# Kernel optimization log

Measured on AMD Instinct MI355X. Metric: run time of the kernel, lower is better.

The kernel has to match this reference:

```python
import jax, jax.numpy as jnp
import numpy as np

NEG_SLOPE = 0.01  # torch F.leaky_relu default

def leaky_relu(x):
    return jnp.where(x >= 0, x, NEG_SLOPE * x)

def setup_inputs() -> dict:
    key = jax.random.key(0)
    ks = jax.random.split(key, 16)
    N, D, H, L = 2048, 512, 256, 16
    # normalized-adjacency-like matrix: row sums ~0.5 to keep activations sane
    A_hat = jax.random.uniform(ks[0], (N, N), dtype=jnp.float32) / N
    X = jax.random.normal(ks[1], (N, D), dtype=jnp.float32)
    eps = jax.random.normal(ks[2], (N, L), dtype=jnp.float32)
    def lin(k, fan_out, fan_in):
        s = 1.0 / np.sqrt(fan_in)
        kw, kb = jax.random.split(k)
        W = jax.random.uniform(kw, (fan_out, fan_in), minval=-s, maxval=s, dtype=jnp.float32)
        b = jax.random.uniform(kb, (fan_out,), minval=-s, maxval=s, dtype=jnp.float32)
        return W, b
    W1, b1 = lin(ks[3], H, D)          # gcn1
    Wmu, bmu = lin(ks[4], L, H)        # gcn2_mu
    Wlv, blv = lin(ks[5], L, H)        # gcn2_logvar
    Wd1, bd1 = lin(ks[6], 2 * L, 2 * L)  # decoder_fc1
    Wd2, bd2 = lin(ks[7], 1, 2 * L)      # decoder_fc2
    return {"A_hat": A_hat, "X": X, "eps": eps,
            "W1": W1, "b1": b1, "Wmu": Wmu, "bmu": bmu,
            "Wlv": Wlv, "blv": blv, "Wd1": Wd1, "bd1": bd1,
            "Wd2": Wd2, "bd2": bd2}

def reference(A_hat, X, eps, W1, b1, Wmu, bmu, Wlv, blv, Wd1, bd1, Wd2, bd2):
    L = Wmu.shape[0]
    # --- encode: two GCN layers (A_hat @ X) @ W.T + b ---
    Hh = leaky_relu((A_hat @ X) @ W1.T + b1)           # [N, H]
    AH = A_hat @ Hh                                    # [N, H]
    mu = AH @ Wmu.T + bmu                              # [N, L]
    logvar = AH @ Wlv.T + blv                          # [N, L]
    # --- reparameterize ---
    Z = mu + eps * jnp.exp(0.5 * logvar)               # [N, L]
    # --- decode: pairwise MLP on concat(Z_i, Z_j), vectorized ---
    # fc1(concat(Zi,Zj)) = Zi @ Wd1[:, :L].T + Zj @ Wd1[:, L:].T + bd1
    P = Z @ Wd1[:, :L].T                               # [N, 2L]
    Q = Z @ Wd1[:, L:].T                               # [N, 2L]
    h = leaky_relu(P[:, None, :] + Q[None, :, :] + bd1)  # [N, N, 2L]
    A_pred = jax.nn.sigmoid(jnp.einsum('nmh,h->nm', h, Wd2[0]) + bd2[0])  # [N, N]
    return (A_pred, mu, logvar)
```

## Files before the change

### kernel.cpp

```cpp
#include <hip/hip_runtime.h>

#define NNODE 2048
#define DD    512
#define HHID  256
#define LLAT  16
#define H2    32

typedef __attribute__((ext_vector_type(8))) short  short8;
typedef __attribute__((ext_vector_type(4))) float  f32x4;

__device__ __forceinline__ unsigned short f2bf(float x) {
    unsigned int u = __float_as_uint(x);
    unsigned int r = (u + 0x7fffu + ((u >> 16) & 1u)) >> 16;
    return (unsigned short)r;
}
__device__ __forceinline__ float bf2f(unsigned short u) {
    return __uint_as_float(((unsigned int)u) << 16);
}

__global__ __launch_bounds__(256) void t0_cvt(const float* __restrict__ A,
                                              const float* __restrict__ X,
                                              const float* __restrict__ W1,
                                              unsigned short* __restrict__ Abf,
                                              unsigned short* __restrict__ Xbf,
                                              unsigned short* __restrict__ W1bf) {
    const int NT = 1343488;
    for (int v = blockIdx.x * 256 + threadIdx.x; v < NT; v += gridDim.x * 256) {
        const float* src; unsigned short* dst; int off;
        if (v < 1048576)      { src = A;  dst = Abf;  off = v; }
        else if (v < 1310720) { src = X;  dst = Xbf;  off = v - 1048576; }
        else                  { src = W1; dst = W1bf; off = v - 1310720; }
        float4 f = ((const float4*)src)[off];
        short4 h;
        h.x = (short)f2bf(f.x); h.y = (short)f2bf(f.y);
        h.z = (short)f2bf(f.z); h.w = (short)f2bf(f.w);
        ((short4*)dst)[off] = h;
    }
}

__global__ __launch_bounds__(256) void t1_full(const unsigned short* __restrict__ W1bf,
                                               const unsigned short* __restrict__ Xbf,
                                               unsigned short* __restrict__ XWt) {
    __shared__ __align__(16) unsigned short Ab[32][72];
    __shared__ __align__(16) unsigned short Bb[32][72];
    const int tid = threadIdx.x;
    const int n0 = blockIdx.x * 32;
    const int h0 = blockIdx.y * 32;
    const int lane = tid & 63, wave = tid >> 6;
    const int wm = wave >> 1, wn = wave & 1;
    const int lm = lane & 15, lk = (lane >> 4) * 8;
    const int sr = tid >> 3, sc = (tid & 7) * 8;
    f32x4 acc = {};
    for (int it = 0; it < 8; ++it) {
        int kk = it * 64;
        *(uint4*)&Ab[sr][sc] = *(const uint4*)(W1bf + (size_t)(h0 + sr) * DD + kk + sc);
        *(uint4*)&Bb[sr][sc] = *(const uint4*)(Xbf  + (size_t)(n0 + sr) * DD + kk + sc);
        __syncthreads();
        #pragma unroll
        for (int ko = 0; ko < 2; ++ko) {
            short8 a = *(const short8*)&Ab[wm * 16 + lm][ko * 32 + lk];
            short8 b = *(const short8*)&Bb[wn * 16 + lm][ko * 32 + lk];
            acc = __builtin_amdgcn_mfma_f32_16x16x32_bf16(a, b, acc, 0, 0, 0);
        }
        __syncthreads();
    }
    #pragma unroll
    for (int r = 0; r < 4; ++r) {
        int row = h0 + wm * 16 + (lane >> 4) * 4 + r;
        int col = n0 + wn * 16 + lm;
        XWt[(size_t)row * NNODE + col] = f2bf(acc[r]);
    }
}

__global__ __launch_bounds__(256) void t2_mfma(const unsigned short* __restrict__ Abf,
                                               const unsigned short* __restrict__ XWt,
                                               float* __restrict__ Hp) {
    __shared__ __align__(16) unsigned short Ab[64][40];
    __shared__ __align__(16) unsigned short Bb[64][40];
    const int tid = threadIdx.x;
    const int m0 = blockIdx.x * 64;
    const int n0 = blockIdx.y * 64;
    const int ks = blockIdx.z;
    const int lane = tid & 63, wave = tid >> 6;
    const int wm = wave >> 1, wn = wave & 1;
    const int lm = lane & 15, lk = (lane >> 4) * 8;
    const int sr = tid >> 2, sc = (tid & 3) * 8;
    f32x4 acc[2][2] = {};
    for (int it = 0; it < 16; ++it) {
        int kk = ks * 512 + it * 32;
        *(uint4*)&Ab[sr][sc] = *(const uint4*)(Abf + (size_t)(m0 + sr) * NNODE + kk + sc);
        *(uint4*)&Bb[sr][sc] = *(const uint4*)(XWt + (size_t)(n0 + sr) * NNODE + kk + sc);
        __syncthreads();
        short8 a0 = *(const short8*)&Ab[wm * 32 + lm][lk];
        short8 a1 = *(const short8*)&Ab[wm * 32 + 16 + lm][lk];
        short8 b0 = *(const short8*)&Bb[wn * 32 + lm][lk];
        short8 b1 = *(const short8*)&Bb[wn * 32 + 16 + lm][lk];
        acc[0][0] = __builtin_amdgcn_mfma_f32_16x16x32_bf16(a0, b0, acc[0][0], 0, 0, 0);
        acc[0][1] = __builtin_amdgcn_mfma_f32_16x16x32_bf16(a0, b1, acc[0][1], 0, 0, 0);
        acc[1][0] = __builtin_amdgcn_mfma_f32_16x16x32_bf16(a1, b0, acc[1][0], 0, 0, 0);
        acc[1][1] = __builtin_amdgcn_mfma_f32_16x16x32_bf16(a1, b1, acc[1][1], 0, 0, 0);
        __syncthreads();
    }
    float* outp = Hp + (size_t)ks * 524288;
    #pragma unroll
    for (int mi = 0; mi < 2; ++mi)
        #pragma unroll
        for (int ni = 0; ni < 2; ++ni)
            #pragma unroll
            for (int r = 0; r < 4; ++r) {
                int row = m0 + wm * 32 + mi * 16 + (lane >> 4) * 4 + r;
                int col = n0 + wn * 32 + ni * 16 + lm;
                outp[(size_t)row * HHID + col] = acc[mi][ni][r];
            }
}

__global__ __launch_bounds__(256) void t3h(const float* __restrict__ Hp,
                                           const float* __restrict__ b1,
                                           const float* __restrict__ Wmu,
                                           const float* __restrict__ Wlv,
                                           unsigned short* __restrict__ Gt) {
    __shared__ float Hs[8][260];
    __shared__ float Ws[32][260];
    const int tid = threadIdx.x;
    const int n0 = blockIdx.x * 8;
    #pragma unroll
    for (int s = 0; s < 8; ++s) {
        int idx = tid + s * 256;
        int row = idx >> 6, c = (idx & 63) * 4;
        const float* src = (row < 16) ? (Wmu + (size_t)row * HHID)
                                      : (Wlv + (size_t)(row - 16) * HHID);
        *(float4*)&Ws[row][c] = *(const float4*)(src + c);
    }
    {
        int r = tid >> 5, seg = tid & 31;
        int dcol = seg * 8;
        const float* base = Hp + (size_t)(n0 + r) * HHID + dcol;
        #pragma unroll
        for (int q = 0; q < 2; ++q) {
            float4 a = *(const float4*)(base + q * 4);
            float4 b = *(const float4*)(base + 524288 + q * 4);
            float4 c = *(const float4*)(base + 1048576 + q * 4);
            float4 e = *(const float4*)(base + 1572864 + q * 4);
            float4 bb = *(const float4*)(b1 + dcol + q * 4);
            float4 s;
            s.x = (a.x + b.x) + (c.x + e.x) + bb.x;
            s.y = (a.y + b.y) + (c.y + e.y) + bb.y;
            s.z = (a.z + b.z) + (c.z + e.z) + bb.z;
            s.w = (a.w + b.w) + (c.w + e.w) + bb.w;
            s.x = fmaxf(s.x, 0.01f * s.x);
            s.y = fmaxf(s.y, 0.01f * s.y);
            s.z = fmaxf(s.z, 0.01f * s.z);
            s.w = fmaxf(s.w, 0.01f * s.w);
            Hs[r][dcol + q * 4 + 0] = bf2f(f2bf(s.x));
            Hs[r][dcol + q * 4 + 1] = bf2f(f2bf(s.y));
            Hs[r][dcol + q * 4 + 2] = bf2f(f2bf(s.z));
            Hs[r][dcol + q * 4 + 3] = bf2f(f2bf(s.w));
        }
    }
    __syncthreads();
    const int r = tid >> 5, j = tid & 31;
    float acc = 0.f;
    #pragma unroll 8
    for (int d4 = 0; d4 < 64; ++d4) {
        float4 a = *(const float4*)&Hs[r][d4 * 4];
        float4 b = *(const float4*)&Ws[j][d4 * 4];
        acc += a.x * b.x + a.y * b.y + a.z * b.z + a.w * b.w;
    }
    Gt[(size_t)j * NNODE + n0 + r] = f2bf(acc);
}

__global__ __launch_bounds__(256) void t4_mfma(const unsigned short* __restrict__ Abf,
                                               const unsigned short* __restrict__ Gt,
                                               float* __restrict__ Mp) {
    __shared__ __align__(16) unsigned short Ab[64][40];
    __shared__ __align__(16) unsigned short Bb[32][40];
    const int tid = threadIdx.x;
    const int m0 = blockIdx.x * 64;
    const int ks = blockIdx.y;
    const int lane = tid & 63, wave = tid >> 6;
    const int lm = lane & 15, lk = (lane >> 4) * 8;
    const int sr = tid >> 2, sc = (tid & 3) * 8;
    f32x4 acc[2] = {};
    for (int it = 0; it < 8; ++it) {
        int kk = ks * 256 + it * 32;
        *(uint4*)&Ab[sr][sc] = *(const uint4*)(Abf + (size_t)(m0 + sr) * NNODE + kk + sc);
        if (tid < 128) {
            int row = tid >> 2, c = (tid & 3) * 8;
            *(uint4*)&Bb[row][c] = *(const uint4*)(Gt + (size_t)row * NNODE + kk + c);
        }
        __syncthreads();
        short8 a  = *(const short8*)&Ab[wave * 16 + lm][lk];
        short8 b0 = *(const short8*)&Bb[lm][lk];
        short8 b1 = *(const short8*)&Bb[16 + lm][lk];
        acc[0] = __builtin_amdgcn_mfma_f32_16x16x32_bf16(a, b0, acc[0], 0, 0, 0);
        acc[1] = __builtin_amdgcn_mfma_f32_16x16x32_bf16(a, b1, acc[1], 0, 0, 0);
        __syncthreads();
    }
    float* outp = Mp + (size_t)ks * 65536;
    #pragma unroll
    for (int ni = 0; ni < 2; ++ni)
        #pragma unroll
        for (int r = 0; r < 4; ++r) {
            int row = m0 + wave * 16 + (lane >> 4) * 4 + r;
            int col = ni * 16 + lm;
            outp[(size_t)row * H2 + col] = acc[ni][r];
        }
}

__global__ __launch_bounds__(256) void t5_z(const float* __restrict__ Mp,
                                            const float* __restrict__ bmu,
                                            const float* __restrict__ blv,
                                            const float* __restrict__ eps,
                                            const float* __restrict__ Wd1,
                                            const float* __restrict__ bd1,
                                            const float* __restrict__ Wd2,
                                            float* __restrict__ out_mu,
                                            float* __restrict__ out_lv,
                                            float* __restrict__ Pp,
                                            float* __restrict__ Qq,
                                            float* __restrict__ WP,
                                            float* __restrict__ WQ) {
    __shared__ float Zs[16][16];
    __shared__ float Psh[16][32];
    __shared__ float Qsh[16][32];
    const int tid = threadIdx.x;
    const int n0 = blockIdx.x * 16;
    {
        int nl = tid >> 4, l = tid & 15;
        int n = n0 + nl;
        float m = bmu[l], lv = blv[l];
        #pragma unroll
        for (int s = 0; s < 8; ++s) {
            m  += Mp[(size_t)s * 65536 + (size_t)n * H2 + l];
            lv += Mp[(size_t)s * 65536 + (size_t)n * H2 + 16 + l];
        }
        out_mu[(size_t)n * LLAT + l] = m;
        out_lv[(size_t)n * LLAT + l] = lv;
        Zs[nl][l] = m + eps[(size_t)n * LLAT + l] * __expf(0.5f * lv);
    }
    __syncthreads();
    #pragma unroll
    for (int p = 0; p < 2; ++p) {
        int idx = tid + p * 256;
        int nl = idx >> 5, o = idx & 31;
        int n = n0 + nl;
        float ap = bd1[o], aq = 0.f;
        #pragma unroll
        for (int l = 0; l < 16; ++l) {
            float z = Zs[nl][l];
            ap = fmaf(z, Wd1[o * H2 + l],      ap);
            aq = fmaf(z, Wd1[o * H2 + 16 + l], aq);
        }
        Pp[(size_t)n * H2 + o] = ap;
        Qq[(size_t)n * H2 + o] = aq;
        Psh[nl][o] = ap;
        Qsh[nl][o] = aq;
    }
    __syncthreads();
    if (tid < 32) {
        int nl = tid & 15, sel = tid >> 4;
        float a = 0.f;
        if (sel == 0) {
            #pragma unroll
            for (int o = 0; o < 32; ++o) a = fmaf(Wd2[o], Psh[nl][o], a);
            WP[n0 + nl] = a;
        } else {
            #pragma unroll
            for (int o = 0; o < 32; ++o) a = fmaf(Wd2[o], Qsh[nl][o], a);
            WQ[n0 + nl] = a;
        }
    }
}

__global__ __launch_bounds__(256) void t6_dec(const float* __restrict__ Pp,
                                              const float* __restrict__ Qq,
                                              const float* __restrict__ WP,
                                              const float* __restrict__ WQ,
                                              const float* __restrict__ Wd2,
                                              const float* __restrict__ bd2,
                                              float* __restrict__ Apred) {
    __shared__ float Qt[32][68];
    __shared__ float Ws2[32];
    __shared__ float WQs[64];
    const int tid = threadIdx.x;
    const int j0 = blockIdx.x * 64, i0 = blockIdx.y * 16;
    #pragma unroll
    for (int s = 0; s < 8; ++s) {
        int idx = tid + s * 256;
        int j = idx >> 5, o = idx & 31;
        Qt[o][j] = Qq[(size_t)(j0 + j) * H2 + o];
    }
    if (tid < 32) Ws2[tid] = Wd2[tid];
    if (tid >= 64 && tid < 128) WQs[tid - 64] = WQ[j0 + tid - 64];
    const int i = i0 + (tid >> 4);
    const int jq = tid & 15;
    float p[32];
    const float4* P4 = (const float4*)(Pp + (size_t)i * H2);
    #pragma unroll
    for (int c = 0; c < 8; ++c) {
        float4 v = P4[c];
        p[c * 4] = v.x; p[c * 4 + 1] = v.y; p[c * 4 + 2] = v.z; p[c * 4 + 3] = v.w;
    }
    const float WPi = WP[i];
    __syncthreads();
    f32x4 acc = {0.f, 0.f, 0.f, 0.f};
    #pragma unroll
    for (int o = 0; o < 32; ++o) {
        float4 q = *(const float4*)&Qt[o][jq * 4];
        float w = Ws2[o], po = p[o];
        acc[0] = fmaf(w, fabsf(po + q.x), acc[0]);
        acc[1] = fmaf(w, fabsf(po + q.y), acc[1]);
        acc[2] = fmaf(w, fabsf(po + q.z), acc[2]);
        acc[3] = fmaf(w, fabsf(po + q.w), acc[3]);
    }
    float4 wq = *(const float4*)&WQs[jq * 4];
    const float base = fmaf(0.505f, WPi, bd2[0]);
    float4 r;
    float l0 = fmaf(0.505f, wq.x, fmaf(0.495f, acc[0], base));
    float l1 = fmaf(0.505f, wq.y, fmaf(0.495f, acc[1], base));
    float l2 = fmaf(0.505f, wq.z, fmaf(0.495f, acc[2], base));
    float l3 = fmaf(0.505f, wq.w, fmaf(0.495f, acc[3], base));
    r.x = 1.f / (1.f + __expf(-l0));
    r.y = 1.f / (1.f + __expf(-l1));
    r.z = 1.f / (1.f + __expf(-l2));
    r.w = 1.f / (1.f + __expf(-l3));
    *(float4*)(Apred + (size_t)i * NNODE + j0 + jq * 4) = r;
}

extern "C" void kernel_launch(void* const* d_in, const int* in_sizes, int n_in,
                              void* d_out, int out_size, void* d_ws, size_t ws_size,
                              hipStream_t stream) {
    const float* A   = (const float*)d_in[0];
    const float* X   = (const float*)d_in[1];
    const float* eps = (const float*)d_in[2];
    const float* W1  = (const float*)d_in[3];
    const float* b1  = (const float*)d_in[4];
    const float* Wmu = (const float*)d_in[5];
    const float* bmu = (const float*)d_in[6];
    const float* Wlv = (const float*)d_in[7];
    const float* blv = (const float*)d_in[8];
    const float* Wd1 = (const float*)d_in[9];
    const float* bd1 = (const float*)d_in[10];
    const float* Wd2 = (const float*)d_in[11];
    const float* bd2 = (const float*)d_in[12];
    float* out = (float*)d_out;
    char* ws = (char*)d_ws;

    unsigned short* Abf  = (unsigned short*)(ws);
    unsigned short* Xbf  = (unsigned short*)(ws + 8388608);
    unsigned short* W1bf = (unsigned short*)(ws + 10485760);
    unsigned short* XWt  = (unsigned short*)(ws + 10747904);
    float*          Hp   = (float*)(ws + 11796480);
    unsigned short* Gt   = (unsigned short*)(ws + 20185088);
    float*          Mp   = (float*)(ws + 20316160);
    float*          Pp   = (float*)(ws + 22413312);
    float*          Qq   = (float*)(ws + 22675456);
    float*          WP   = (float*)(ws + 22937600);
    float*          WQ   = (float*)(ws + 22945792);

    float* out_mu = out + (size_t)NNODE * NNODE;
    float* out_lv = out_mu + NNODE * LLAT;

    t0_cvt <<<2048,            256, 0, stream>>>(A, X, W1, Abf, Xbf, W1bf);
    t1_full<<<dim3(64, 8),     256, 0, stream>>>(W1bf, Xbf, XWt);
    t2_mfma<<<dim3(32, 4, 4),  256, 0, stream>>>(Abf, XWt, Hp);
    t3h    <<<256,             256, 0, stream>>>(Hp, b1, Wmu, Wlv, Gt);
    t4_mfma<<<dim3(32, 8),     256, 0, stream>>>(Abf, Gt, Mp);
    t5_z   <<<128,             256, 0, stream>>>(Mp, bmu, blv, eps, Wd1, bd1, Wd2,
                                                 out_mu, out_lv, Pp, Qq, WP, WQ);
    t6_dec <<<dim3(32, 128),   256, 0, stream>>>(Pp, Qq, WP, WQ, Wd2, bd2, out);
}
```

Measured before the change: 137.1 us.

## Replace split-K GEMM with full-K tile, fusing bias and leaky ReLU

The second GEMM (A_hat times XW) no longer splits K four ways into fp32 partial buffers that a later kernel sums. Each block now covers the full K=2048 on a smaller 32x32 tile and applies bias and leaky ReLU in its epilogue, writing bf16 H directly. Global loads are register-prefetched one iteration ahead. This removes the 8MB fp32 partial writes and reads. In exchange, each block runs a longer serial K loop and does less work per LDS load, with 512 blocks instead of 512 split-K blocks.

```diff
diff --git a/kernel.cpp b/kernel.cpp
--- a/kernel.cpp
+++ b/kernel.cpp
@@ -72,53 +72,55 @@
     }
 }
 
-__global__ __launch_bounds__(256) void t2_mfma(const unsigned short* __restrict__ Abf,
+__global__ __launch_bounds__(256) void t2_full(const unsigned short* __restrict__ Abf,
                                                const unsigned short* __restrict__ XWt,
-                                               float* __restrict__ Hp) {
-    __shared__ __align__(16) unsigned short Ab[64][40];
-    __shared__ __align__(16) unsigned short Bb[64][40];
-    const int tid = threadIdx.x;
-    const int m0 = blockIdx.x * 64;
-    const int n0 = blockIdx.y * 64;
-    const int ks = blockIdx.z;
+                                               const float* __restrict__ bias1,
+                                               unsigned short* __restrict__ Hbf) {
+    __shared__ __align__(16) unsigned short Ab[32][72];
+    __shared__ __align__(16) unsigned short Bb[32][72];
+    const int tid = threadIdx.x;
+    const int m0 = blockIdx.x * 32;
+    const int h0 = blockIdx.y * 32;
     const int lane = tid & 63, wave = tid >> 6;
     const int wm = wave >> 1, wn = wave & 1;
     const int lm = lane & 15, lk = (lane >> 4) * 8;
-    const int sr = tid >> 2, sc = (tid & 3) * 8;
-    f32x4 acc[2][2] = {};
-    for (int it = 0; it < 16; ++it) {
-        int kk = ks * 512 + it * 32;
-        *(uint4*)&Ab[sr][sc] = *(const uint4*)(Abf + (size_t)(m0 + sr) * NNODE + kk + sc);
-        *(uint4*)&Bb[sr][sc] = *(const uint4*)(XWt + (size_t)(n0 + sr) * NNODE + kk + sc);
-        __syncthreads();
-        short8 a0 = *(const short8*)&Ab[wm * 32 + lm][lk];
-        short8 a1 = *(const short8*)&Ab[wm * 32 + 16 + lm][lk];
-        short8 b0 = *(const short8*)&Bb[wn * 32 + lm][lk];
-        short8 b1 = *(const short8*)&Bb[wn * 32 + 16 + lm][lk];
-        acc[0][0] = __builtin_amdgcn_mfma_f32_16x16x32_bf16(a0, b0, acc[0][0], 0, 0, 0);
-        acc[0][1] = __builtin_amdgcn_mfma_f32_16x16x32_bf16(a0, b1, acc[0][1], 0, 0, 0);
-        acc[1][0] = __builtin_amdgcn_mfma_f32_16x16x32_bf16(a1, b0, acc[1][0], 0, 0, 0);
-        acc[1][1] = __builtin_amdgcn_mfma_f32_16x16x32_bf16(a1, b1, acc[1][1], 0, 0, 0);
-        __syncthreads();
-    }
-    float* outp = Hp + (size_t)ks * 524288;
-    #pragma unroll
-    for (int mi = 0; mi < 2; ++mi)
-        #pragma unroll
-        for (int ni = 0; ni < 2; ++ni)
-            #pragma unroll
-            for (int r = 0; r < 4; ++r) {
-                int row = m0 + wm * 32 + mi * 16 + (lane >> 4) * 4 + r;
-                int col = n0 + wn * 32 + ni * 16 + lm;
-                outp[(size_t)row * HHID + col] = acc[mi][ni][r];
-            }
-}
-
-__global__ __launch_bounds__(256) void t3h(const float* __restrict__ Hp,
-                                           const float* __restrict__ b1,
-                                           const float* __restrict__ Wmu,
-                                           const float* __restrict__ Wlv,
-                                           unsigned short* __restrict__ Gt) {
+    const int sr = tid >> 3, sc = (tid & 7) * 8;
+    const unsigned short* aA = Abf + (size_t)(m0 + sr) * NNODE + sc;
+    const unsigned short* aB = XWt + (size_t)(h0 + sr) * NNODE + sc;
+    uint4 ra = *(const uint4*)aA;
+    uint4 rb = *(const uint4*)aB;
+    f32x4 acc = {};
+    for (int it = 0; it < 32; ++it) {
+        *(uint4*)&Ab[sr][sc] = ra;
+        *(uint4*)&Bb[sr][sc] = rb;
+        __syncthreads();
+        if (it < 31) {
+            ra = *(const uint4*)(aA + (it + 1) * 64);
+            rb = *(const uint4*)(aB + (it + 1) * 64);
+        }
+        #pragma unroll
+        for (int ko = 0; ko < 2; ++ko) {
+            short8 a = *(const short8*)&Ab[wm * 16 + lm][ko * 32 + lk];
+            short8 b = *(const short8*)&Bb[wn * 16 + lm][ko * 32 + lk];
+            acc = __builtin_amdgcn_mfma_f32_16x16x32_bf16(a, b, acc, 0, 0, 0);
+        }
+        __syncthreads();
+    }
+    const int col = h0 + wn * 16 + lm;
+    const float bb = bias1[col];
+    #pragma unroll
+    for (int r = 0; r < 4; ++r) {
+        int row = m0 + wm * 16 + (lane >> 4) * 4 + r;
+        float s = acc[r] + bb;
+        s = fmaxf(s, 0.01f * s);
+        Hbf[(size_t)row * HHID + col] = f2bf(s);
+    }
+}
+
+__global__ __launch_bounds__(256) void t3_g(const unsigned short* __restrict__ Hbf,
+                                            const float* __restrict__ Wmu,
+                                            const float* __restrict__ Wlv,
+                                            unsigned short* __restrict__ Gt) {
     __shared__ float Hs[8][260];
     __shared__ float Ws[32][260];
     const int tid = threadIdx.x;
@@ -133,29 +135,13 @@
     }
     {
         int r = tid >> 5, seg = tid & 31;
-        int dcol = seg * 8;
-        const float* base = Hp + (size_t)(n0 + r) * HHID + dcol;
-        #pragma unroll
-        for (int q = 0; q < 2; ++q) {
-            float4 a = *(const float4*)(base + q * 4);
-            float4 b = *(const float4*)(base + 524288 + q * 4);
-            float4 c = *(const float4*)(base + 1048576 + q * 4);
-            float4 e = *(const float4*)(base + 1572864 + q * 4);
-            float4 bb = *(const float4*)(b1 + dcol + q * 4);
-            float4 s;
-            s.x = (a.x + b.x) + (c.x + e.x) + bb.x;
-            s.y = (a.y + b.y) + (c.y + e.y) + bb.y;
-            s.z = (a.z + b.z) + (c.z + e.z) + bb.z;
-            s.w = (a.w + b.w) + (c.w + e.w) + bb.w;
-            s.x = fmaxf(s.x, 0.01f * s.x);
-            s.y = fmaxf(s.y, 0.01f * s.y);
-            s.z = fmaxf(s.z, 0.01f * s.z);
-            s.w = fmaxf(s.w, 0.01f * s.w);
-            Hs[r][dcol + q * 4 + 0] = bf2f(f2bf(s.x));
-            Hs[r][dcol + q * 4 + 1] = bf2f(f2bf(s.y));
-            Hs[r][dcol + q * 4 + 2] = bf2f(f2bf(s.z));
-            Hs[r][dcol + q * 4 + 3] = bf2f(f2bf(s.w));
-        }
+        int d = seg * 8;
+        ushort4 u0 = *(const ushort4*)(Hbf + (size_t)(n0 + r) * HHID + d);
+        ushort4 u1 = *(const ushort4*)(Hbf + (size_t)(n0 + r) * HHID + d + 4);
+        Hs[r][d + 0] = bf2f(u0.x); Hs[r][d + 1] = bf2f(u0.y);
+        Hs[r][d + 2] = bf2f(u0.z); Hs[r][d + 3] = bf2f(u0.w);
+        Hs[r][d + 4] = bf2f(u1.x); Hs[r][d + 5] = bf2f(u1.y);
+        Hs[r][d + 6] = bf2f(u1.z); Hs[r][d + 7] = bf2f(u1.w);
     }
     __syncthreads();
     const int r = tid >> 5, j = tid & 31;
@@ -350,21 +336,21 @@
     unsigned short* Xbf  = (unsigned short*)(ws + 8388608);
     unsigned short* W1bf = (unsigned short*)(ws + 10485760);
     unsigned short* XWt  = (unsigned short*)(ws + 10747904);
-    float*          Hp   = (float*)(ws + 11796480);
-    unsigned short* Gt   = (unsigned short*)(ws + 20185088);
-    float*          Mp   = (float*)(ws + 20316160);
-    float*          Pp   = (float*)(ws + 22413312);
-    float*          Qq   = (float*)(ws + 22675456);
-    float*          WP   = (float*)(ws + 22937600);
-    float*          WQ   = (float*)(ws + 22945792);
+    unsigned short* Hbf  = (unsigned short*)(ws + 11796480);
+    unsigned short* Gt   = (unsigned short*)(ws + 12845056);
+    float*          Mp   = (float*)(ws + 12976128);
+    float*          Pp   = (float*)(ws + 15073280);
+    float*          Qq   = (float*)(ws + 15335424);
+    float*          WP   = (float*)(ws + 15597568);
+    float*          WQ   = (float*)(ws + 15605760);
 
     float* out_mu = out + (size_t)NNODE * NNODE;
     float* out_lv = out_mu + NNODE * LLAT;
 
     t0_cvt <<<2048,            256, 0, stream>>>(A, X, W1, Abf, Xbf, W1bf);
     t1_full<<<dim3(64, 8),     256, 0, stream>>>(W1bf, Xbf, XWt);
-    t2_mfma<<<dim3(32, 4, 4),  256, 0, stream>>>(Abf, XWt, Hp);
-    t3h    <<<256,             256, 0, stream>>>(Hp, b1, Wmu, Wlv, Gt);
+    t2_full<<<dim3(64, 8),     256, 0, stream>>>(Abf, XWt, b1, Hbf);
+    t3_g   <<<256,             256, 0, stream>>>(Hbf, Wmu, Wlv, Gt);
     t4_mfma<<<dim3(32, 8),     256, 0, stream>>>(Abf, Gt, Mp);
     t5_z   <<<128,             256, 0, stream>>>(Mp, bmu, blv, eps, Wd1, bd1, Wd2,
                                                  out_mu, out_lv, Pp, Qq, WP, WQ);
```

Result: slower. 144.7 us (+5.6%).
